# Performance work log

Measured on AMD Instinct MI355X. Metric: run time of the kernel, lower is better.

## Reference

```python
import jax, jax.numpy as jnp
import numpy as np

N_NODES = 50000
N_EDGES = 1_600_000
IN_FEAT = 128
OUT_FEAT = 128
NUM_RELS = 16


def setup_inputs() -> dict:
    key = jax.random.key(0)
    k_h, k_w, k_src, k_dst, k_rel = jax.random.split(key, 5)
    h = jax.random.normal(k_h, (N_NODES, IN_FEAT), dtype=jnp.float32)
    # xavier_uniform with relu gain ~ sqrt(2) * sqrt(6/(in+out))
    gain = np.sqrt(2.0)
    bound = gain * np.sqrt(6.0 / (IN_FEAT + OUT_FEAT))
    weight = jax.random.uniform(k_w, (NUM_RELS, IN_FEAT, OUT_FEAT),
                                dtype=jnp.float32, minval=-bound, maxval=bound)
    bias = jnp.zeros((OUT_FEAT,), dtype=jnp.float32)
    src = jax.random.randint(k_src, (N_EDGES,), 0, N_NODES, dtype=jnp.int32)
    dst = jax.random.randint(k_dst, (N_EDGES,), 0, N_NODES, dtype=jnp.int32)
    rel_type = jax.random.randint(k_rel, (N_EDGES,), 0, NUM_RELS, dtype=jnp.int32)
    return {"h": h, "weight": weight, "bias": bias,
            "src": src, "dst": dst, "rel_type": rel_type}


def reference(h, weight, bias, src, dst, rel_type):
    # Transform every node by every relation weight once: [R, N, out]
    # (equivalent to per-edge bmm h[src] @ weight[rel], but avoids an
    #  [E, in, out] weight gather)
    hw = jnp.einsum('ni,rio->rno', h, weight)
    # Per-edge message: msg[e] = h[src[e]] @ weight[rel_type[e]]  -> [E, out]
    msg = hw[rel_type, src]
    # Scatter-sum aggregation to destination nodes: [N, out]
    agg = jax.ops.segment_sum(msg, dst, num_segments=h.shape[0])
    # apply_func: bias + relu
    out = jax.nn.relu(agg + bias)
    return out
```

## Files before the change

### kernel.cpp

```cpp
#include <hip/hip_runtime.h>
#include <hip/hip_bf16.h>
#include <stdint.h>

typedef __attribute__((ext_vector_type(8))) short short8_t;
typedef __attribute__((ext_vector_type(4))) float f32x4;
typedef __attribute__((ext_vector_type(4))) int   i32x4;

#define AS1 __attribute__((address_space(1)))
#define AS3 __attribute__((address_space(3)))

#define CB_SHIFT 9
#define CBUCK 512
#define FCHUNK 6144
#define PADSLACK 4096

__device__ __forceinline__ void gload_lds16(const void* g, void* l) {
    __builtin_amdgcn_global_load_lds((const AS1 unsigned int*)g,
                                     (AS3 unsigned int*)l, 16, 0, 0);
}

__device__ __forceinline__ unsigned short f2bf(float f) {
    unsigned int u = __float_as_uint(f);
    unsigned int r = (u + 0x7FFFu + ((u >> 16) & 1u)) >> 16;
    return (unsigned short)r;
}

__global__ void prep_kernel(const float* __restrict__ h,
                            unsigned short* __restrict__ hb,
                            const float* __restrict__ w,
                            unsigned short* __restrict__ wt,
                            const int* __restrict__ dst,
                            int* __restrict__ cnt,
                            unsigned int* __restrict__ zrow,
                            int total4, int total4p, int castBlocks,
                            int R, int nE, int nseg) {
    __shared__ int hist[128];
    const int b = blockIdx.x;
    if (b < castBlocks) {
        int t = b * 256 + threadIdx.x;
        if (t < total4) {
            float4 v = ((const float4*)h)[t];
            ushort4 o;
            o.x = f2bf(v.x); o.y = f2bf(v.y); o.z = f2bf(v.z); o.w = f2bf(v.w);
            *(ushort4*)(hb + (size_t)t * 4) = o;
        } else if (t < total4p) {
            *(ushort4*)(hb + (size_t)t * 4) = make_ushort4(0, 0, 0, 0);
        }
        return;
    }
    if (b < castBlocks + R) {
        int r = b - castBlocks;
        const float* wr = w + (size_t)r * 16384;
        unsigned short* wtr = wt + (size_t)r * 16384;
        for (int x = threadIdx.x; x < 16384; x += blockDim.x) {
            int i = x >> 7, o = x & 127;
            wtr[o * 128 + i] = f2bf(wr[x]);
        }
        return;
    }
    if (b < castBlocks + R + 256) {
        if (threadIdx.x < 128) hist[threadIdx.x] = 0;
        __syncthreads();
        int b2 = b - castBlocks - R;
        for (int e = b2 * 256 + threadIdx.x; e < nE; e += 65536)
            atomicAdd(&hist[dst[e] >> CB_SHIFT], 1);
        __syncthreads();
        if (threadIdx.x < nseg) {
            int v = hist[threadIdx.x];
            if (v) atomicAdd(cnt + threadIdx.x, v);
        }
        return;
    }
    if (threadIdx.x < 64) zrow[threadIdx.x] = 0u;
}

__global__ __launch_bounds__(512, 4) void binGemm_kernel(
    const int* __restrict__ cnt, const int* __restrict__ packed,
    int* __restrict__ packed2, int2* __restrict__ s2e2,
    int nseg, int zrow, int binBlocks,
    const unsigned short* __restrict__ hb,
    const unsigned short* __restrict__ wt,
    unsigned short* __restrict__ hw,
    int r0, int rc, int np, int nwg)
{
    __shared__ __align__(16) char smem[65536];
    const int tid = threadIdx.x;

    if (blockIdx.x < (unsigned)binBlocks) {
        int* hist = (int*)smem;
        int* pscn = hist + CBUCK;
        int* cur  = pscn + CBUCK;
        int* segb = cur + CBUCK;
        const int b = blockIdx.x;
        if (tid < 128) segb[tid] = (tid < nseg) ? cnt[tid] : 0;
        hist[tid] = 0;
        __syncthreads();
        for (int off = 1; off < 128; off <<= 1) {
            int t = 0;
            if (tid < 128 && tid >= off) t = segb[tid - off];
            __syncthreads();
            if (tid < 128) segb[tid] += t;
            __syncthreads();
        }
        const int e0 = segb[b];
        const int s0 = e0 - cnt[b];
        for (int k = s0 + tid; k < e0; k += 512)
            atomicAdd(&hist[(packed[k] >> 20) & (CBUCK - 1)], 1);
        __syncthreads();
        int pc = (hist[tid] + 7) & ~7;
        pscn[tid] = pc;
        __syncthreads();
        for (int off = 1; off < CBUCK; off <<= 1) {
            int t = (tid >= off) ? pscn[tid - off] : 0;
            __syncthreads();
            pscn[tid] += t;
            __syncthreads();
        }
        const int pbase = s0 + b * PADSLACK;
        int ps = pbase + pscn[tid] - pc;
        cur[tid] = ps;
        s2e2[(size_t)b * CBUCK + tid] = make_int2(ps, ps + pc);
        __syncthreads();
        for (int k = s0 + tid; k < e0; k += 512) {
            int pk = packed[k];
            int pos = atomicAdd(&cur[(pk >> 20) & (CBUCK - 1)], 1);
            packed2[pos] = pk;
        }
        __syncthreads();
        int pend = ps + pc;
        for (int p = cur[tid]; p < pend; ++p) packed2[p] = zrow;
        return;
    }

    char* ldsA = smem;
    char* ldsB = smem + 32768;
    const int lane = tid & 63;
    const int wv   = tid >> 6;
    const int wr   = wv >> 1;
    const int wc   = wv & 1;
    const int l15  = lane & 15, kb = lane >> 4;

    const int flat = blockIdx.x - binBlocks;
    const int q = nwg >> 3, rm = nwg & 7;
    const int xcd = flat & 7, ii = flat >> 3;
    const int orig = (xcd < rm ? xcd * (q + 1) : rm * (q + 1) + (xcd - rm) * q) + ii;
    const int rloc = orig % rc;
    const int rowb = orig / rc;
    const int rel  = r0 + rloc;
    const size_t rowBase = (size_t)rowb * 128;

    const char* gA = (const char*)(hb + rowBase * 128);
    const char* gB = (const char*)(wt + (size_t)rel * 16384);

#pragma unroll
    for (int it = 0; it < 4; ++it) {
        int p = it * 8192 + tid * 16;
        int row = p >> 8;
        int so = (row << 8) + ((p & 255) ^ ((row & 7) << 4));
        gload_lds16(gA + so, ldsA + p);
        gload_lds16(gB + so, ldsB + p);
    }
    __syncthreads();

    f32x4 acc[2][4];
#pragma unroll
    for (int m = 0; m < 2; ++m)
#pragma unroll
        for (int n = 0; n < 4; ++n) acc[m][n] = (f32x4){0.f, 0.f, 0.f, 0.f};

#pragma unroll
    for (int kk = 0; kk < 4; ++kk) {
        short8_t a[2], b[4];
#pragma unroll
        for (int m = 0; m < 2; ++m) {
            int row = wr * 32 + m * 16 + l15;
            int byte = row * 256 + ((kk * 64 + kb * 16) ^ ((row & 7) << 4));
            a[m] = *(const short8_t*)(ldsA + byte);
        }
#pragma unroll
        for (int n = 0; n < 4; ++n) {
            int row = wc * 64 + n * 16 + l15;
            int byte = row * 256 + ((kk * 64 + kb * 16) ^ ((row & 7) << 4));
            b[n] = *(const short8_t*)(ldsB + byte);
        }
#pragma unroll
        for (int m = 0; m < 2; ++m)
#pragma unroll
            for (int n = 0; n < 4; ++n)
                acc[m][n] = __builtin_amdgcn_mfma_f32_16x16x32_bf16(
                    a[m], b[n], acc[m][n], 0, 0, 0);
    }

    __syncthreads();
#pragma unroll
    for (int m = 0; m < 2; ++m) {
#pragma unroll
        for (int n = 0; n < 4; ++n) {
            int col = wc * 64 + n * 16 + l15;
#pragma unroll
            for (int j = 0; j < 4; ++j) {
                int row = wr * 32 + m * 16 + kb * 4 + j;
                int byte = row * 256 + ((col * 2) ^ ((row & 7) << 4));
                *(unsigned short*)(smem + byte) = f2bf(acc[m][n][j]);
            }
        }
    }
    __syncthreads();

    char* gC = (char*)(hw + ((size_t)rloc * np + rowBase) * 128);
#pragma unroll
    for (int j = 0; j < 4; ++j) {
        int p = j * 8192 + tid * 16;
        int row = p >> 8;
        i32x4 v = *(const i32x4*)(smem + row * 256 + ((p & 255) ^ ((row & 7) << 4)));
        *(i32x4*)(gC + p) = v;
    }
}

__global__ __launch_bounds__(256) void fill_staged_kernel(
    const int* __restrict__ src, const int* __restrict__ dst,
    const int* __restrict__ rel, const int* __restrict__ cnt,
    int* __restrict__ cur,
    int* __restrict__ packed, int nE, int nseg, int np)
{
    __shared__ int stage[FCHUNK];
    __shared__ int hist[128], lscan[128], lcur[128], gbase[128], segb[128];
    const int tid = threadIdx.x;
    const int e0 = blockIdx.x * FCHUNK;
    const int e1 = min(nE, e0 + FCHUNK);

    if (tid < 128) {
        hist[tid] = 0;
        segb[tid] = (tid < nseg) ? cnt[tid] : 0;
    }
    __syncthreads();
    for (int off = 1; off < 128; off <<= 1) {
        int t = 0;
        if (tid < 128 && tid >= off) t = segb[tid - off];
        __syncthreads();
        if (tid < 128) segb[tid] += t;
        __syncthreads();
    }
    if (tid < 128) segb[tid] -= (tid < nseg) ? cnt[tid] : 0;

    for (int e = e0 + tid; e < e1; e += 256)
        atomicAdd(&hist[dst[e] >> CB_SHIFT], 1);
    __syncthreads();

    if (tid < 128) lscan[tid] = hist[tid];
    __syncthreads();
    for (int off = 1; off < 128; off <<= 1) {
        int t = 0;
        if (tid < 128 && tid >= off) t = lscan[tid - off];
        __syncthreads();
        if (tid < 128) lscan[tid] += t;
        __syncthreads();
    }
    if (tid < 128) {
        int excl = lscan[tid] - hist[tid];
        lcur[tid] = excl;
        lscan[tid] = excl;
        gbase[tid] = segb[tid] +
            ((tid < nseg && hist[tid]) ? atomicAdd(cur + tid, hist[tid]) : 0);
    }
    __syncthreads();

    for (int e = e0 + tid; e < e1; e += 256) {
        int d = dst[e];
        int seg = d >> CB_SHIFT;
        int pk = (rel[e] * np + src[e]) | ((d & (CBUCK - 1)) << 20);
        int lp = atomicAdd(&lcur[seg], 1);
        stage[lp] = pk;
    }
    __syncthreads();

    const int wv = tid >> 6, lane = tid & 63;
    for (int s = wv; s < nseg; s += 4) {
        int n = hist[s], from = lscan[s], to = gbase[s];
        for (int i = lane; i < n; i += 64)
            packed[to + i] = stage[from + i];
    }
}

__global__ __launch_bounds__(256) void gather2_kernel(
    const unsigned short* __restrict__ hw,
    const int2* __restrict__ s2e2,
    const int* __restrict__ packed2,
    const float* __restrict__ bias,
    float* __restrict__ outp, float* __restrict__ agg,
    int n, int r0np, int rcnp, int zrl, int flags )
{
    int wid  = (blockIdx.x * blockDim.x + threadIdx.x) >> 6;
    int lane = threadIdx.x & 63;
    if (wid >= n) return;
    int2 se = s2e2[wid];
    int s = se.x, e = se.y;
    float a0 = 0.f, a1 = 0.f, a2 = 0.f, a3 = 0.f;
    const uint2* hw8 = (const uint2*)hw;
    const int half = lane >> 5;
    const int c0 = lane & 31;

    for (int base = s; base < e; base += 64) {
        int m = e - base; if (m > 64) m = 64;
        int myp = (base + lane < e) ? packed2[base + lane] : 0;
        for (int k = 0; k < m; k += 8) {
            uint2 v[4];
#pragma unroll
            for (int t = 0; t < 4; ++t) {
                int pe = __shfl(myp, k + 2 * t + half);
                int rl = (pe & 0xFFFFF) - r0np;
                if ((unsigned)rl >= (unsigned)rcnp) rl = zrl;
                v[t] = hw8[(size_t)rl * 32 + c0];
            }
#pragma unroll
            for (int t = 0; t < 4; ++t) {
                a0 += __uint_as_float(v[t].x << 16);
                a1 += __uint_as_float(v[t].x & 0xFFFF0000u);
                a2 += __uint_as_float(v[t].y << 16);
                a3 += __uint_as_float(v[t].y & 0xFFFF0000u);
            }
        }
    }
    a0 += __shfl_xor(a0, 32);
    a1 += __shfl_xor(a1, 32);
    a2 += __shfl_xor(a2, 32);
    a3 += __shfl_xor(a3, 32);

    if (lane < 32) {
        float4 acc4 = make_float4(a0, a1, a2, a3);
        float* ap = agg + (size_t)wid * 128 + c0 * 4;
        if (!(flags & 1)) {
            float4 p = *(const float4*)ap;
            acc4.x += p.x; acc4.y += p.y; acc4.z += p.z; acc4.w += p.w;
        }
        if (flags & 2) {
            float4 bv = *(const float4*)(bias + c0 * 4);
            float4 o;
            o.x = fmaxf(acc4.x + bv.x, 0.f);
            o.y = fmaxf(acc4.y + bv.y, 0.f);
            o.z = fmaxf(acc4.z + bv.z, 0.f);
            o.w = fmaxf(acc4.w + bv.w, 0.f);
            *(float4*)(outp + (size_t)wid * 128 + c0 * 4) = o;
        } else {
            *(float4*)ap = acc4;
        }
    }
}

static inline size_t align256(size_t x) { return (x + 255) & ~(size_t)255; }

extern "C" void kernel_launch(void* const* d_in, const int* in_sizes, int n_in,
                              void* d_out, int out_size, void* d_ws, size_t ws_size,
                              hipStream_t stream) {
    const float* h    = (const float*)d_in[0];
    const float* w    = (const float*)d_in[1];
    const float* bias = (const float*)d_in[2];
    const int*   src  = (const int*)d_in[3];
    const int*   dst  = (const int*)d_in[4];
    const int*   rel  = (const int*)d_in[5];
    float* out = (float*)d_out;

    const int N  = in_sizes[0] / 128;
    const int E  = in_sizes[3];
    const int R  = in_sizes[1] / (128 * 128);
    const int NB = (N + 127) / 128;
    const int NP = NB * 128;
    const int NSEG = (N + CBUCK - 1) >> CB_SHIFT;

    char* ws = (char*)d_ws;
    size_t off = 0;
    unsigned short* hb = (unsigned short*)(ws + off);
    off = align256(off + (size_t)NP * 128 * 2);
    unsigned short* wt = (unsigned short*)(ws + off);
    off = align256(off + (size_t)R * 16384 * 2);
    int* cntA = (int*)(ws + off);
    off = align256(off + 128 * 4);
    int* curA = (int*)(ws + off);
    off = align256(off + 128 * 4);
    int2* s2e2A = (int2*)(ws + off);
    off = align256(off + (size_t)NSEG * CBUCK * 8);
    int* packed = (int*)(ws + off);
    off = align256(off + (size_t)E * 4);
    int* packed2 = (int*)(ws + off);
    off = align256(off + ((size_t)E + (size_t)NSEG * PADSLACK + 64) * 4);
    size_t fixed = off;

    size_t perRel = (size_t)NP * 128 * 2;
    size_t aggB   = (size_t)N * 128 * 4;
    size_t avail  = ws_size > fixed ? ws_size - fixed : 0;

    int RC, fused; float* agg; unsigned short* hwb;
    if (avail >= (size_t)R * perRel + 256) {
        RC = R; fused = 1;
        hwb = (unsigned short*)(ws + fixed);
        agg = (float*)(ws + fixed);
    } else {
        fused = 0;
        agg = (float*)(ws + fixed);
        size_t a2 = avail > aggB + 256 ? avail - aggB - 256 : 0;
        RC = (int)(a2 / perRel);
        if (RC > R) RC = R;
        if (RC < 1) RC = 1;
        hwb = (unsigned short*)(ws + align256(fixed + aggB));
    }

    hipMemsetAsync(cntA, 0, align256(128 * 4) + 128 * 4, stream);

    int total4  = N * 32;
    int total4p = NP * 32;
    int castBlocks = (total4p + 255) / 256;
    int prepBlocks = castBlocks + R + 256 + 1;
    prep_kernel<<<prepBlocks, 256, 0, stream>>>(
        h, hb, w, wt, dst, cntA,
        (unsigned int*)(hwb + (size_t)RC * NP * 128),
        total4, total4p, castBlocks, R, E, NSEG);

    fill_staged_kernel<<<(E + FCHUNK - 1) / FCHUNK, 256, 0, stream>>>(
        src, dst, rel, cntA, curA, packed, E, NSEG, NP);

    int gblocks = (N * 64 + 255) / 256;
    for (int r0 = 0; r0 < R; r0 += RC) {
        int rc = (R - r0 < RC) ? (R - r0) : RC;
        int nwg = NB * rc;
        int binBlocks = (r0 == 0) ? NSEG : 0;
        binGemm_kernel<<<binBlocks + nwg, 512, 0, stream>>>(
            cntA, packed, packed2, s2e2A, NSEG, R * NP, binBlocks,
            hb, wt, hwb, r0, rc, NP, nwg);
        int flags = (r0 == 0 ? 1 : 0) | (r0 + rc >= R ? 2 : 0);
        gather2_kernel<<<gblocks, 256, 0, stream>>>(hwb, s2e2A, packed2, bias,
                                                    out, agg, N, r0 * NP,
                                                    rc * NP, RC * NP,
                                                    fused ? 3 : flags);
    }
}
```

Measured before the change: 202.1 us.

## Split relations into chunks and pipeline GEMM with gather in one mega kernel

Relations are split into four chunks. Edges are binned by (relation chunk, dst bucket) with wider 2048-node buckets. A single mega kernel per step runs the binning, the GEMM for chunk c into a double buffer, and the gather for chunk c-1, so the transform and aggregation stages overlap and the hw buffer stays small. The gather now skips empty nodes in middle chunks and no longer needs per-edge relation range checks. The cost is an extra pass over agg per chunk, more launches and more complex indexing.

```diff
diff --git a/kernel.cpp b/kernel.cpp
--- a/kernel.cpp
+++ b/kernel.cpp
@@ -9,10 +9,11 @@
 #define AS1 __attribute__((address_space(1)))
 #define AS3 __attribute__((address_space(3)))
 
-#define CB_SHIFT 9
-#define CBUCK 512
+#define CB2_SHIFT 11
+#define CBUCK2 2048
 #define FCHUNK 6144
-#define PADSLACK 4096
+#define PADSLACK2 16384
+#define NCHUNKS 4
 
 __device__ __forceinline__ void gload_lds16(const void* g, void* l) {
     __builtin_amdgcn_global_load_lds((const AS1 unsigned int*)g,
@@ -30,10 +31,12 @@
                             const float* __restrict__ w,
                             unsigned short* __restrict__ wt,
                             const int* __restrict__ dst,
+                            const int* __restrict__ rel,
                             int* __restrict__ cnt,
-                            unsigned int* __restrict__ zrow,
+                            unsigned int* __restrict__ z0,
+                            unsigned int* __restrict__ z1,
                             int total4, int total4p, int castBlocks,
-                            int R, int nE, int nseg) {
+                            int R, int nE, int nseg2, int ncb, int rpc) {
     __shared__ int hist[128];
     const int b = blockIdx.x;
     if (b < castBlocks) {
@@ -62,38 +65,115 @@
         if (threadIdx.x < 128) hist[threadIdx.x] = 0;
         __syncthreads();
         int b2 = b - castBlocks - R;
-        for (int e = b2 * 256 + threadIdx.x; e < nE; e += 65536)
-            atomicAdd(&hist[dst[e] >> CB_SHIFT], 1);
-        __syncthreads();
-        if (threadIdx.x < nseg) {
+        for (int e = b2 * 256 + threadIdx.x; e < nE; e += 65536) {
+            int seg = (rel[e] / rpc) * ncb + (dst[e] >> CB2_SHIFT);
+            atomicAdd(&hist[seg], 1);
+        }
+        __syncthreads();
+        if (threadIdx.x < nseg2) {
             int v = hist[threadIdx.x];
             if (v) atomicAdd(cnt + threadIdx.x, v);
         }
         return;
     }
-    if (threadIdx.x < 64) zrow[threadIdx.x] = 0u;
-}
-
-__global__ __launch_bounds__(512, 4) void binGemm_kernel(
+    if (threadIdx.x < 64) { z0[threadIdx.x] = 0u; z1[threadIdx.x] = 0u; }
+}
+
+__global__ __launch_bounds__(256) void fill_staged_kernel(
+    const int* __restrict__ src, const int* __restrict__ dst,
+    const int* __restrict__ rel, const int* __restrict__ cnt,
+    int* __restrict__ cur,
+    int* __restrict__ packed, int nE, int nseg2, int ncb, int rpc, int np)
+{
+    __shared__ int stage[FCHUNK];
+    __shared__ int hist[128], lscan[128], lcur[128], gbase[128], segb[128];
+    const int tid = threadIdx.x;
+    const int e0 = blockIdx.x * FCHUNK;
+    const int e1 = min(nE, e0 + FCHUNK);
+
+    if (tid < 128) {
+        hist[tid] = 0;
+        segb[tid] = (tid < nseg2) ? cnt[tid] : 0;
+    }
+    __syncthreads();
+    for (int off = 1; off < 128; off <<= 1) {
+        int t = 0;
+        if (tid < 128 && tid >= off) t = segb[tid - off];
+        __syncthreads();
+        if (tid < 128) segb[tid] += t;
+        __syncthreads();
+    }
+    if (tid < 128) segb[tid] -= (tid < nseg2) ? cnt[tid] : 0;
+
+    for (int e = e0 + tid; e < e1; e += 256) {
+        int seg = (rel[e] / rpc) * ncb + (dst[e] >> CB2_SHIFT);
+        atomicAdd(&hist[seg], 1);
+    }
+    __syncthreads();
+
+    if (tid < 128) lscan[tid] = hist[tid];
+    __syncthreads();
+    for (int off = 1; off < 128; off <<= 1) {
+        int t = 0;
+        if (tid < 128 && tid >= off) t = lscan[tid - off];
+        __syncthreads();
+        if (tid < 128) lscan[tid] += t;
+        __syncthreads();
+    }
+    if (tid < 128) {
+        int excl = lscan[tid] - hist[tid];
+        lcur[tid] = excl;
+        lscan[tid] = excl;
+        gbase[tid] = segb[tid] +
+            ((tid < nseg2 && hist[tid]) ? atomicAdd(cur + tid, hist[tid]) : 0);
+    }
+    __syncthreads();
+
+    for (int e = e0 + tid; e < e1; e += 256) {
+        int d = dst[e], r = rel[e];
+        int chunk = r / rpc;
+        int seg = chunk * ncb + (d >> CB2_SHIFT);
+        int pk = ((r - chunk * rpc) * np + src[e]) | ((d & (CBUCK2 - 1)) << 18);
+        int lp = atomicAdd(&lcur[seg], 1);
+        stage[lp] = pk;
+    }
+    __syncthreads();
+
+    const int wv = tid >> 6, lane = tid & 63;
+    for (int s = wv; s < nseg2; s += 4) {
+        int n = hist[s], from = lscan[s], to = gbase[s];
+        for (int i = lane; i < n; i += 64)
+            packed[to + i] = stage[from + i];
+    }
+}
+
+__global__ __launch_bounds__(512, 4) void mega_kernel(
+    int binBlocks, int gemmBlocks,
     const int* __restrict__ cnt, const int* __restrict__ packed,
     int* __restrict__ packed2, int2* __restrict__ s2e2,
-    int nseg, int zrow, int binBlocks,
+    int nseg2, int ncb, int zrow,
     const unsigned short* __restrict__ hb,
     const unsigned short* __restrict__ wt,
-    unsigned short* __restrict__ hw,
-    int r0, int rc, int np, int nwg)
+    unsigned short* __restrict__ hwW,
+    int relBase, int rc, int np, int nwg,
+    const unsigned short* __restrict__ hwR,
+    const float* __restrict__ bias,
+    float* __restrict__ outp, float* __restrict__ agg,
+    int n, int gchunk, int flags)
 {
     __shared__ __align__(16) char smem[65536];
     const int tid = threadIdx.x;
-
-    if (blockIdx.x < (unsigned)binBlocks) {
+    const int bid = blockIdx.x;
+
+    if (bid < (unsigned)binBlocks) {
         int* hist = (int*)smem;
-        int* pscn = hist + CBUCK;
-        int* cur  = pscn + CBUCK;
-        int* segb = cur + CBUCK;
-        const int b = blockIdx.x;
-        if (tid < 128) segb[tid] = (tid < nseg) ? cnt[tid] : 0;
-        hist[tid] = 0;
+        int* curp = hist + CBUCK2;
+        int* aux  = curp + CBUCK2;
+        int* segb = aux + 512;
+        const int b2 = bid;
+        const int chunk = b2 / ncb, cb = b2 - chunk * ncb;
+        for (int i = tid; i < CBUCK2; i += 512) hist[i] = 0;
+        if (tid < 128) segb[tid] = (tid < nseg2) ? cnt[tid] : 0;
         __syncthreads();
         for (int off = 1; off < 128; off <<= 1) {
             int t = 0;
@@ -102,215 +182,166 @@
             if (tid < 128) segb[tid] += t;
             __syncthreads();
         }
-        const int e0 = segb[b];
-        const int s0 = e0 - cnt[b];
+        const int e0 = segb[b2];
+        const int s0 = e0 - cnt[b2];
+        __syncthreads();
         for (int k = s0 + tid; k < e0; k += 512)
-            atomicAdd(&hist[(packed[k] >> 20) & (CBUCK - 1)], 1);
-        __syncthreads();
-        int pc = (hist[tid] + 7) & ~7;
-        pscn[tid] = pc;
-        __syncthreads();
-        for (int off = 1; off < CBUCK; off <<= 1) {
-            int t = (tid >= off) ? pscn[tid - off] : 0;
+            atomicAdd(&hist[(packed[k] >> 18) & (CBUCK2 - 1)], 1);
+        __syncthreads();
+        const int base4 = tid * 4;
+        int pc[4], ssum = 0;
+#pragma unroll
+        for (int j = 0; j < 4; ++j) {
+            pc[j] = (hist[base4 + j] + 7) & ~7;
+            ssum += pc[j];
+        }
+        aux[tid] = ssum;
+        __syncthreads();
+        int acc = ssum;
+        for (int off = 1; off < 512; off <<= 1) {
+            int t = (tid >= off) ? aux[tid - off] : 0;
             __syncthreads();
-            pscn[tid] += t;
+            acc += t; aux[tid] = acc;
             __syncthreads();
         }
-        const int pbase = s0 + b * PADSLACK;
-        int ps = pbase + pscn[tid] - pc;
-        cur[tid] = ps;
-        s2e2[(size_t)b * CBUCK + tid] = make_int2(ps, ps + pc);
+        int run = s0 + b2 * PADSLACK2 + (acc - ssum);
+#pragma unroll
+        for (int j = 0; j < 4; ++j) {
+            int node = (cb << CB2_SHIFT) + base4 + j;
+            curp[base4 + j] = run;
+            int endp = run + pc[j];
+            if (node < n)
+                s2e2[(size_t)chunk * n + node] = make_int2(run, endp);
+            run = endp;
+        }
+        __syncthreads();
+#pragma unroll
+        for (int j = 0; j < 4; ++j)
+            hist[base4 + j] = curp[base4 + j] + pc[j];
         __syncthreads();
         for (int k = s0 + tid; k < e0; k += 512) {
             int pk = packed[k];
-            int pos = atomicAdd(&cur[(pk >> 20) & (CBUCK - 1)], 1);
-            packed2[pos] = pk;
-        }
-        __syncthreads();
-        int pend = ps + pc;
-        for (int p = cur[tid]; p < pend; ++p) packed2[p] = zrow;
+            int pos = atomicAdd(&curp[(pk >> 18) & (CBUCK2 - 1)], 1);
+            packed2[pos] = pk & 0x3FFFF;
+        }
+        __syncthreads();
+#pragma unroll
+        for (int j = 0; j < 4; ++j) {
+            int pend = hist[base4 + j];
+            for (int p = curp[base4 + j]; p < pend; ++p) packed2[p] = zrow;
+        }
         return;
     }
 
-    char* ldsA = smem;
-    char* ldsB = smem + 32768;
+    if (bid < (unsigned)(binBlocks + gemmBlocks)) {
+        char* ldsA = smem;
+        char* ldsB = smem + 32768;
+        const int lane = tid & 63;
+        const int wv   = tid >> 6;
+        const int wr   = wv >> 1;
+        const int wc   = wv & 1;
+        const int l15  = lane & 15, kb = lane >> 4;
+
+        const int flat = bid - binBlocks;
+        const int q = nwg >> 3, rm = nwg & 7;
+        const int xcd = flat & 7, ii = flat >> 3;
+        const int orig = (xcd < rm ? xcd * (q + 1) : rm * (q + 1) + (xcd - rm) * q) + ii;
+        const int rloc = orig % rc;
+        const int rowb = orig / rc;
+        const int rel  = relBase + rloc;
+        const size_t rowBase = (size_t)rowb * 128;
+
+        const char* gA = (const char*)(hb + rowBase * 128);
+        const char* gB = (const char*)(wt + (size_t)rel * 16384);
+
+#pragma unroll
+        for (int it = 0; it < 4; ++it) {
+            int p = it * 8192 + tid * 16;
+            int row = p >> 8;
+            int so = (row << 8) + ((p & 255) ^ ((row & 7) << 4));
+            gload_lds16(gA + so, ldsA + p);
+            gload_lds16(gB + so, ldsB + p);
+        }
+        __syncthreads();
+
+        f32x4 acc[2][4];
+#pragma unroll
+        for (int m = 0; m < 2; ++m)
+#pragma unroll
+            for (int nn = 0; nn < 4; ++nn) acc[m][nn] = (f32x4){0.f, 0.f, 0.f, 0.f};
+
+#pragma unroll
+        for (int kk = 0; kk < 4; ++kk) {
+            short8_t a[2], b[4];
+#pragma unroll
+            for (int m = 0; m < 2; ++m) {
+                int row = wr * 32 + m * 16 + l15;
+                int byte = row * 256 + ((kk * 64 + kb * 16) ^ ((row & 7) << 4));
+                a[m] = *(const short8_t*)(ldsA + byte);
+            }
+#pragma unroll
+            for (int nn = 0; nn < 4; ++nn) {
+                int row = wc * 64 + nn * 16 + l15;
+                int byte = row * 256 + ((kk * 64 + kb * 16) ^ ((row & 7) << 4));
+                b[nn] = *(const short8_t*)(ldsB + byte);
+            }
+#pragma unroll
+            for (int m = 0; m < 2; ++m)
+#pragma unroll
+                for (int nn = 0; nn < 4; ++nn)
+                    acc[m][nn] = __builtin_amdgcn_mfma_f32_16x16x32_bf16(
+                        a[m], b[nn], acc[m][nn], 0, 0, 0);
+        }
+
+        __syncthreads();
+#pragma unroll
+        for (int m = 0; m < 2; ++m) {
+#pragma unroll
+            for (int nn = 0; nn < 4; ++nn) {
+                int col = wc * 64 + nn * 16 + l15;
+#pragma unroll
+                for (int j = 0; j < 4; ++j) {
+                    int row = wr * 32 + m * 16 + kb * 4 + j;
+                    int byte = row * 256 + ((col * 2) ^ ((row & 7) << 4));
+                    *(unsigned short*)(smem + byte) = f2bf(acc[m][nn][j]);
+                }
+            }
+        }
+        __syncthreads();
+
+        char* gC = (char*)(hwW + ((size_t)rloc * np + rowBase) * 128);
+#pragma unroll
+        for (int j = 0; j < 4; ++j) {
+            int p = j * 8192 + tid * 16;
+            int row = p >> 8;
+            i32x4 v = *(const i32x4*)(smem + row * 256 + ((p & 255) ^ ((row & 7) << 4)));
+            *(i32x4*)(gC + p) = v;
+        }
+        return;
+    }
+
     const int lane = tid & 63;
     const int wv   = tid >> 6;
-    const int wr   = wv >> 1;
-    const int wc   = wv & 1;
-    const int l15  = lane & 15, kb = lane >> 4;
-
-    const int flat = blockIdx.x - binBlocks;
-    const int q = nwg >> 3, rm = nwg & 7;
-    const int xcd = flat & 7, ii = flat >> 3;
-    const int orig = (xcd < rm ? xcd * (q + 1) : rm * (q + 1) + (xcd - rm) * q) + ii;
-    const int rloc = orig % rc;
-    const int rowb = orig / rc;
-    const int rel  = r0 + rloc;
-    const size_t rowBase = (size_t)rowb * 128;
-
-    const char* gA = (const char*)(hb + rowBase * 128);
-    const char* gB = (const char*)(wt + (size_t)rel * 16384);
-
-#pragma unroll
-    for (int it = 0; it < 4; ++it) {
-        int p = it * 8192 + tid * 16;
-        int row = p >> 8;
-        int so = (row << 8) + ((p & 255) ^ ((row & 7) << 4));
-        gload_lds16(gA + so, ldsA + p);
-        gload_lds16(gB + so, ldsB + p);
-    }
-    __syncthreads();
-
-    f32x4 acc[2][4];
-#pragma unroll
-    for (int m = 0; m < 2; ++m)
-#pragma unroll
-        for (int n = 0; n < 4; ++n) acc[m][n] = (f32x4){0.f, 0.f, 0.f, 0.f};
-
-#pragma unroll
-    for (int kk = 0; kk < 4; ++kk) {
-        short8_t a[2], b[4];
-#pragma unroll
-        for (int m = 0; m < 2; ++m) {
-            int row = wr * 32 + m * 16 + l15;
-            int byte = row * 256 + ((kk * 64 + kb * 16) ^ ((row & 7) << 4));
-            a[m] = *(const short8_t*)(ldsA + byte);
-        }
-#pragma unroll
-        for (int n = 0; n < 4; ++n) {
-            int row = wc * 64 + n * 16 + l15;
-            int byte = row * 256 + ((kk * 64 + kb * 16) ^ ((row & 7) << 4));
-            b[n] = *(const short8_t*)(ldsB + byte);
-        }
-#pragma unroll
-        for (int m = 0; m < 2; ++m)
-#pragma unroll
-            for (int n = 0; n < 4; ++n)
-                acc[m][n] = __builtin_amdgcn_mfma_f32_16x16x32_bf16(
-                    a[m], b[n], acc[m][n], 0, 0, 0);
-    }
-
-    __syncthreads();
-#pragma unroll
-    for (int m = 0; m < 2; ++m) {
-#pragma unroll
-        for (int n = 0; n < 4; ++n) {
-            int col = wc * 64 + n * 16 + l15;
-#pragma unroll
-            for (int j = 0; j < 4; ++j) {
-                int row = wr * 32 + m * 16 + kb * 4 + j;
-                int byte = row * 256 + ((col * 2) ^ ((row & 7) << 4));
-                *(unsigned short*)(smem + byte) = f2bf(acc[m][n][j]);
-            }
-        }
-    }
-    __syncthreads();
-
-    char* gC = (char*)(hw + ((size_t)rloc * np + rowBase) * 128);
-#pragma unroll
-    for (int j = 0; j < 4; ++j) {
-        int p = j * 8192 + tid * 16;
-        int row = p >> 8;
-        i32x4 v = *(const i32x4*)(smem + row * 256 + ((p & 255) ^ ((row & 7) << 4)));
-        *(i32x4*)(gC + p) = v;
-    }
-}
-
-__global__ __launch_bounds__(256) void fill_staged_kernel(
-    const int* __restrict__ src, const int* __restrict__ dst,
-    const int* __restrict__ rel, const int* __restrict__ cnt,
-    int* __restrict__ cur,
-    int* __restrict__ packed, int nE, int nseg, int np)
-{
-    __shared__ int stage[FCHUNK];
-    __shared__ int hist[128], lscan[128], lcur[128], gbase[128], segb[128];
-    const int tid = threadIdx.x;
-    const int e0 = blockIdx.x * FCHUNK;
-    const int e1 = min(nE, e0 + FCHUNK);
-
-    if (tid < 128) {
-        hist[tid] = 0;
-        segb[tid] = (tid < nseg) ? cnt[tid] : 0;
-    }
-    __syncthreads();
-    for (int off = 1; off < 128; off <<= 1) {
-        int t = 0;
-        if (tid < 128 && tid >= off) t = segb[tid - off];
-        __syncthreads();
-        if (tid < 128) segb[tid] += t;
-        __syncthreads();
-    }
-    if (tid < 128) segb[tid] -= (tid < nseg) ? cnt[tid] : 0;
-
-    for (int e = e0 + tid; e < e1; e += 256)
-        atomicAdd(&hist[dst[e] >> CB_SHIFT], 1);
-    __syncthreads();
-
-    if (tid < 128) lscan[tid] = hist[tid];
-    __syncthreads();
-    for (int off = 1; off < 128; off <<= 1) {
-        int t = 0;
-        if (tid < 128 && tid >= off) t = lscan[tid - off];
-        __syncthreads();
-        if (tid < 128) lscan[tid] += t;
-        __syncthreads();
-    }
-    if (tid < 128) {
-        int excl = lscan[tid] - hist[tid];
-        lcur[tid] = excl;
-        lscan[tid] = excl;
-        gbase[tid] = segb[tid] +
-            ((tid < nseg && hist[tid]) ? atomicAdd(cur + tid, hist[tid]) : 0);
-    }
-    __syncthreads();
-
-    for (int e = e0 + tid; e < e1; e += 256) {
-        int d = dst[e];
-        int seg = d >> CB_SHIFT;
-        int pk = (rel[e] * np + src[e]) | ((d & (CBUCK - 1)) << 20);
-        int lp = atomicAdd(&lcur[seg], 1);
-        stage[lp] = pk;
-    }
-    __syncthreads();
-
-    const int wv = tid >> 6, lane = tid & 63;
-    for (int s = wv; s < nseg; s += 4) {
-        int n = hist[s], from = lscan[s], to = gbase[s];
-        for (int i = lane; i < n; i += 64)
-            packed[to + i] = stage[from + i];
-    }
-}
-
-__global__ __launch_bounds__(256) void gather2_kernel(
-    const unsigned short* __restrict__ hw,
-    const int2* __restrict__ s2e2,
-    const int* __restrict__ packed2,
-    const float* __restrict__ bias,
-    float* __restrict__ outp, float* __restrict__ agg,
-    int n, int r0np, int rcnp, int zrl, int flags )
-{
-    int wid  = (blockIdx.x * blockDim.x + threadIdx.x) >> 6;
-    int lane = threadIdx.x & 63;
+    int wid = (bid - binBlocks - gemmBlocks) * 8 + wv;
     if (wid >= n) return;
-    int2 se = s2e2[wid];
+    int2 se = s2e2[(size_t)gchunk * n + wid];
     int s = se.x, e = se.y;
+    const bool mid = !(flags & 3);
+    if (s == e && mid) return;
     float a0 = 0.f, a1 = 0.f, a2 = 0.f, a3 = 0.f;
-    const uint2* hw8 = (const uint2*)hw;
+    const uint2* hw8 = (const uint2*)hwR;
     const int half = lane >> 5;
     const int c0 = lane & 31;
 
     for (int base = s; base < e; base += 64) {
         int m = e - base; if (m > 64) m = 64;
-        int myp = (base + lane < e) ? packed2[base + lane] : 0;
+        int myp = (base + lane < e) ? packed2[base + lane] : zrow;
         for (int k = 0; k < m; k += 8) {
             uint2 v[4];
 #pragma unroll
             for (int t = 0; t < 4; ++t) {
                 int pe = __shfl(myp, k + 2 * t + half);
-                int rl = (pe & 0xFFFFF) - r0np;
-                if ((unsigned)rl >= (unsigned)rcnp) rl = zrl;
-                v[t] = hw8[(size_t)rl * 32 + c0];
+                v[t] = hw8[(size_t)pe * 32 + c0];
             }
 #pragma unroll
             for (int t = 0; t < 4; ++t) {
@@ -365,7 +396,11 @@
     const int R  = in_sizes[1] / (128 * 128);
     const int NB = (N + 127) / 128;
     const int NP = NB * 128;
-    const int NSEG = (N + CBUCK - 1) >> CB_SHIFT;
+    int CH = NCHUNKS; if (CH > R) CH = R;
+    const int RPC = (R + CH - 1) / CH;
+    const int NCB = (N + CBUCK2 - 1) >> CB2_SHIFT;
+    const int nseg2 = CH * NCB;
+    const int ZROW = RPC * NP;
 
     char* ws = (char*)d_ws;
     size_t off = 0;
@@ -378,31 +413,16 @@
     int* curA = (int*)(ws + off);
     off = align256(off + 128 * 4);
     int2* s2e2A = (int2*)(ws + off);
-    off = align256(off + (size_t)NSEG * CBUCK * 8);
+    off = align256(off + (size_t)CH * N * 8);
     int* packed = (int*)(ws + off);
     off = align256(off + (size_t)E * 4);
     int* packed2 = (int*)(ws + off);
-    off = align256(off + ((size_t)E + (size_t)NSEG * PADSLACK + 64) * 4);
-    size_t fixed = off;
-
-    size_t perRel = (size_t)NP * 128 * 2;
-    size_t aggB   = (size_t)N * 128 * 4;
-    size_t avail  = ws_size > fixed ? ws_size - fixed : 0;
-
-    int RC, fused; float* agg; unsigned short* hwb;
-    if (avail >= (size_t)R * perRel + 256) {
-        RC = R; fused = 1;
-        hwb = (unsigned short*)(ws + fixed);
-        agg = (float*)(ws + fixed);
-    } else {
-        fused = 0;
-        agg = (float*)(ws + fixed);
-        size_t a2 = avail > aggB + 256 ? avail - aggB - 256 : 0;
-        RC = (int)(a2 / perRel);
-        if (RC > R) RC = R;
-        if (RC < 1) RC = 1;
-        hwb = (unsigned short*)(ws + align256(fixed + aggB));
-    }
+    off = align256(off + ((size_t)E + (size_t)nseg2 * PADSLACK2 + 64) * 4);
+    float* agg = (float*)(ws + off);
+    off = align256(off + (size_t)N * 128 * 4);
+    size_t bufB = align256(((size_t)RPC * NP + 1) * 128 * 2);
+    unsigned short* buf0 = (unsigned short*)(ws + off); off += bufB;
+    unsigned short* buf1 = (unsigned short*)(ws + off); off += bufB;
 
     hipMemsetAsync(cntA, 0, align256(128 * 4) + 128 * 4, stream);
 
@@ -411,25 +431,28 @@
     int castBlocks = (total4p + 255) / 256;
     int prepBlocks = castBlocks + R + 256 + 1;
     prep_kernel<<<prepBlocks, 256, 0, stream>>>(
-        h, hb, w, wt, dst, cntA,
-        (unsigned int*)(hwb + (size_t)RC * NP * 128),
-        total4, total4p, castBlocks, R, E, NSEG);
+        h, hb, w, wt, dst, rel, cntA,
+        (unsigned int*)(buf0 + (size_t)ZROW * 128),
+        (unsigned int*)(buf1 + (size_t)ZROW * 128),
+        total4, total4p, castBlocks, R, E, nseg2, NCB, RPC);
 
     fill_staged_kernel<<<(E + FCHUNK - 1) / FCHUNK, 256, 0, stream>>>(
-        src, dst, rel, cntA, curA, packed, E, NSEG, NP);
-
-    int gblocks = (N * 64 + 255) / 256;
-    for (int r0 = 0; r0 < R; r0 += RC) {
-        int rc = (R - r0 < RC) ? (R - r0) : RC;
-        int nwg = NB * rc;
-        int binBlocks = (r0 == 0) ? NSEG : 0;
-        binGemm_kernel<<<binBlocks + nwg, 512, 0, stream>>>(
-            cntA, packed, packed2, s2e2A, NSEG, R * NP, binBlocks,
-            hb, wt, hwb, r0, rc, NP, nwg);
-        int flags = (r0 == 0 ? 1 : 0) | (r0 + rc >= R ? 2 : 0);
-        gather2_kernel<<<gblocks, 256, 0, stream>>>(hwb, s2e2A, packed2, bias,
-                                                    out, agg, N, r0 * NP,
-                                                    rc * NP, RC * NP,
-                                                    fused ? 3 : flags);
-    }
-}
+        src, dst, rel, cntA, curA, packed, E, nseg2, NCB, RPC, NP);
+
+    unsigned short* bufs[2] = {buf0, buf1};
+    const int gatherBlocks = (N + 7) / 8;
+    for (int c = 0; c <= CH; ++c) {
+        int rcC   = (c < CH) ? ((R - c * RPC < RPC) ? (R - c * RPC) : RPC) : 0;
+        int gemmB = (c < CH) ? NB * rcC : 0;
+        int binB  = (c == 0) ? nseg2 : 0;
+        int gB    = (c > 0) ? gatherBlocks : 0;
+        int gchunk = c - 1;
+        int flags = (gchunk == 0 ? 1 : 0) | (gchunk == CH - 1 ? 2 : 0);
+        mega_kernel<<<binB + gemmB + gB, 512, 0, stream>>>(
+            binB, gemmB,
+            cntA, packed, packed2, s2e2A, nseg2, NCB, ZROW,
+            hb, wt, bufs[c & 1], c * RPC, rcC < 1 ? 1 : rcC, NP, gemmB,
+            bufs[(c > 0 ? gchunk : 0) & 1], bias, out, agg, N,
+            gchunk < 0 ? 0 : gchunk, flags);
+    }
+}
```

New measurement: 296.5 us. +46.7%, slower.

## Move h/weight bf16 casts into fill kernel and use nontemporal hw stores

Applied to the files above, without the earlier changes.

Moves the h and weight bf16 conversion blocks out of the histogram prep kernel and into the edge-binning fill kernel. The prep kernel now only counts destinations, so it finishes sooner and the cast work overlaps with the edge fill work in one launch. The fill kernel's blocks now hold a large 24KB shared stage buffer even for the cast-only blocks, which may lower occupancy for that work. The GEMM output stores to hw also become nontemporal, to avoid polluting cache with data consumed later by gather.

```diff
diff --git a/kernel.cpp b/kernel.cpp
--- a/kernel.cpp
+++ b/kernel.cpp
@@ -25,44 +25,16 @@
     return (unsigned short)r;
 }
 
-__global__ void prep_kernel(const float* __restrict__ h,
-                            unsigned short* __restrict__ hb,
-                            const float* __restrict__ w,
-                            unsigned short* __restrict__ wt,
-                            const int* __restrict__ dst,
+__global__ void prep_kernel(const int* __restrict__ dst,
                             int* __restrict__ cnt,
                             unsigned int* __restrict__ zrow,
-                            int total4, int total4p, int castBlocks,
-                            int R, int nE, int nseg) {
+                            int nE, int nseg) {
     __shared__ int hist[128];
     const int b = blockIdx.x;
-    if (b < castBlocks) {
-        int t = b * 256 + threadIdx.x;
-        if (t < total4) {
-            float4 v = ((const float4*)h)[t];
-            ushort4 o;
-            o.x = f2bf(v.x); o.y = f2bf(v.y); o.z = f2bf(v.z); o.w = f2bf(v.w);
-            *(ushort4*)(hb + (size_t)t * 4) = o;
-        } else if (t < total4p) {
-            *(ushort4*)(hb + (size_t)t * 4) = make_ushort4(0, 0, 0, 0);
-        }
-        return;
-    }
-    if (b < castBlocks + R) {
-        int r = b - castBlocks;
-        const float* wr = w + (size_t)r * 16384;
-        unsigned short* wtr = wt + (size_t)r * 16384;
-        for (int x = threadIdx.x; x < 16384; x += blockDim.x) {
-            int i = x >> 7, o = x & 127;
-            wtr[o * 128 + i] = f2bf(wr[x]);
-        }
-        return;
-    }
-    if (b < castBlocks + R + 256) {
+    if (b < 256) {
         if (threadIdx.x < 128) hist[threadIdx.x] = 0;
         __syncthreads();
-        int b2 = b - castBlocks - R;
-        for (int e = b2 * 256 + threadIdx.x; e < nE; e += 65536)
+        for (int e = b * 256 + threadIdx.x; e < nE; e += 65536)
             atomicAdd(&hist[dst[e] >> CB_SHIFT], 1);
         __syncthreads();
         if (threadIdx.x < nseg) {
@@ -213,11 +185,14 @@
         int p = j * 8192 + tid * 16;
         int row = p >> 8;
         i32x4 v = *(const i32x4*)(smem + row * 256 + ((p & 255) ^ ((row & 7) << 4)));
-        *(i32x4*)(gC + p) = v;
-    }
-}
-
-__global__ __launch_bounds__(256) void fill_staged_kernel(
+        __builtin_nontemporal_store(v, (i32x4*)(gC + p));
+    }
+}
+
+__global__ __launch_bounds__(256) void fillcast_kernel(
+    const float* __restrict__ h, unsigned short* __restrict__ hb,
+    const float* __restrict__ w, unsigned short* __restrict__ wtp,
+    int total4, int total4p, int castBlocks, int R,
     const int* __restrict__ src, const int* __restrict__ dst,
     const int* __restrict__ rel, const int* __restrict__ cnt,
     int* __restrict__ cur,
@@ -226,7 +201,32 @@
     __shared__ int stage[FCHUNK];
     __shared__ int hist[128], lscan[128], lcur[128], gbase[128], segb[128];
     const int tid = threadIdx.x;
-    const int e0 = blockIdx.x * FCHUNK;
+    const int b = blockIdx.x;
+
+    if (b < castBlocks) {
+        int t = b * 256 + tid;
+        if (t < total4) {
+            float4 v = ((const float4*)h)[t];
+            ushort4 o;
+            o.x = f2bf(v.x); o.y = f2bf(v.y); o.z = f2bf(v.z); o.w = f2bf(v.w);
+            *(ushort4*)(hb + (size_t)t * 4) = o;
+        } else if (t < total4p) {
+            *(ushort4*)(hb + (size_t)t * 4) = make_ushort4(0, 0, 0, 0);
+        }
+        return;
+    }
+    if (b < castBlocks + R) {
+        int r = b - castBlocks;
+        const float* wr = w + (size_t)r * 16384;
+        unsigned short* wtr = wtp + (size_t)r * 16384;
+        for (int x = tid; x < 16384; x += 256) {
+            int i = x >> 7, o = x & 127;
+            wtr[o * 128 + i] = f2bf(wr[x]);
+        }
+        return;
+    }
+
+    const int e0 = (b - castBlocks - R) * FCHUNK;
     const int e1 = min(nE, e0 + FCHUNK);
 
     if (tid < 128) {
@@ -406,16 +406,15 @@
 
     hipMemsetAsync(cntA, 0, align256(128 * 4) + 128 * 4, stream);
 
+    prep_kernel<<<257, 256, 0, stream>>>(
+        dst, cntA, (unsigned int*)(hwb + (size_t)RC * NP * 128), E, NSEG);
+
     int total4  = N * 32;
     int total4p = NP * 32;
     int castBlocks = (total4p + 255) / 256;
-    int prepBlocks = castBlocks + R + 256 + 1;
-    prep_kernel<<<prepBlocks, 256, 0, stream>>>(
-        h, hb, w, wt, dst, cntA,
-        (unsigned int*)(hwb + (size_t)RC * NP * 128),
-        total4, total4p, castBlocks, R, E, NSEG);
-
-    fill_staged_kernel<<<(E + FCHUNK - 1) / FCHUNK, 256, 0, stream>>>(
+    int fillBlocks = (E + FCHUNK - 1) / FCHUNK;
+    fillcast_kernel<<<castBlocks + R + fillBlocks, 256, 0, stream>>>(
+        h, hb, w, wt, total4, total4p, castBlocks, R,
         src, dst, rel, cntA, curA, packed, E, NSEG, NP);
 
     int gblocks = (N * 64 + 255) / 256;
```

Result: faster. 187.7 us (-7.1%).
